# Kernel optimization log

Measured on AMD Instinct MI355X. Metric: run time of the kernel, lower is better.

The kernel has to match this reference:

```python
import jax, jax.numpy as jnp
import numpy as np

BINS = 1024
HEADS = 8
HEAD_DIM = BINS // HEADS          # 128
ROT_DIM = HEAD_DIM // 2           # 64 (rotary applied to first half of head dim)


def depthwise_conv_w(y, kernel):
    # y: (b, c, w, bins); depthwise length-3 conv along frame axis w, pad 1
    b, c, w, g = y.shape
    y2 = y.reshape(b * c, w, g)
    out = jax.lax.conv_general_dilated(
        y2, kernel, window_strides=(1,), padding=((1, 1),),
        dimension_numbers=('NWC', 'WIO', 'NWC'), feature_group_count=g)
    return out.reshape(b, c, w, g)


def rotate_half(x):
    # interleaved pair rotation: (x0,x1) -> (-x1,x0)
    x1 = x[..., ::2]
    x2 = x[..., 1::2]
    return jnp.stack([-x2, x1], axis=-1).reshape(x.shape)


def apply_rotary(t, inv_freq):
    # t: (b, c, H, w, d); rotate first ROT_DIM features along seq axis w
    w = t.shape[-2]
    pos = jnp.arange(w, dtype=t.dtype)
    freqs = pos[:, None] * inv_freq[None, :]        # (w, ROT_DIM//2)
    freqs = jnp.repeat(freqs, 2, axis=-1)           # (w, ROT_DIM)
    cos, sin = jnp.cos(freqs), jnp.sin(freqs)
    t_rot, t_pass = t[..., :ROT_DIM], t[..., ROT_DIM:]
    t_rot = t_rot * cos + rotate_half(t_rot) * sin
    return jnp.concatenate([t_rot, t_pass], axis=-1)


def _qkv(x, W, conv_k):
    # linear over last (bins) dim then depthwise conv over frames, split heads
    y = jnp.einsum('bcwh,gh->bcwg', x, W)
    y = depthwise_conv_w(y, conv_k)
    b, c, w, _ = y.shape
    return y.reshape(b, c, w, HEADS, HEAD_DIM).transpose(0, 1, 3, 2, 4)  # (b,c,H,w,d)


def setup_inputs() -> dict:
    key = jax.random.key(0)
    ks = jax.random.split(key, 8)
    s = 0.02
    inv_freq = (1.0 / (10000.0 ** (np.arange(0, ROT_DIM, 2, dtype=np.float32) / ROT_DIM)))
    return {
        'x': jax.random.normal(ks[0], (2, 2, 1024, BINS), dtype=jnp.float32),
        'q_w': jax.random.normal(ks[1], (BINS, BINS), dtype=jnp.float32) * s,
        'q_conv': jax.random.normal(ks[2], (3, 1, BINS), dtype=jnp.float32) * 0.3,
        'k_w': jax.random.normal(ks[3], (BINS, BINS), dtype=jnp.float32) * s,
        'k_conv': jax.random.normal(ks[4], (3, 1, BINS), dtype=jnp.float32) * 0.3,
        'v_w': jax.random.normal(ks[5], (BINS, BINS), dtype=jnp.float32) * s,
        'v_conv': jax.random.normal(ks[6], (3, 1, BINS), dtype=jnp.float32) * 0.3,
        'out_w': jax.random.normal(ks[7], (BINS, BINS), dtype=jnp.float32) * s,
        'inv_freq': jnp.asarray(inv_freq),
    }


def reference(x, q_w, q_conv, k_w, k_conv, v_w, v_conv, out_w, inv_freq):
    b, c, w, h = x.shape  # h == BINS
    q = apply_rotary(_qkv(x, q_w, q_conv), inv_freq)
    k = apply_rotary(_qkv(x, k_w, k_conv), inv_freq)
    v = _qkv(x, v_w, v_conv)
    scale = 1.0 / jnp.sqrt(jnp.asarray(h, x.dtype))   # NOTE: scale by sqrt(bins), per source
    scores = jnp.einsum('bchqd,bchkd->bchqk', q, k) * scale
    a = jax.nn.softmax(scores, axis=-1)
    o = jnp.einsum('bchqk,bchkd->bchqd', a, v)
    o = o.transpose(0, 1, 3, 2, 4).reshape(b, c, w, h)
    return jnp.einsum('bcwh,gh->bcwg', o, out_w)
```

## Files before the change

### kernel.cpp

```cpp
#include <hip/hip_runtime.h>
#include <stdint.h>

typedef float fv4 __attribute__((ext_vector_type(4)));
typedef float fv2 __attribute__((ext_vector_type(2)));
typedef int   iv4 __attribute__((ext_vector_type(4)));
typedef short sv4 __attribute__((ext_vector_type(4)));
typedef short sv8 __attribute__((ext_vector_type(8)));

__device__ __forceinline__ short f2bf(float f) {
  uint32_t u = __builtin_bit_cast(uint32_t, f);
  u += 0x7FFFu + ((u >> 16) & 1u);
  return (short)(u >> 16);
}
__device__ __forceinline__ float bf2f(short s) {
  uint32_t u = ((uint32_t)(uint16_t)s) << 16;
  return __builtin_bit_cast(float, u);
}
__device__ __forceinline__ float redmax16(float v) {
#pragma unroll
  for (int m = 1; m < 16; m <<= 1) v = fmaxf(v, __shfl_xor(v, m));
  return v;
}
__device__ __forceinline__ float redsum16(float v) {
#pragma unroll
  for (int m = 1; m < 16; m <<= 1) v += __shfl_xor(v, m);
  return v;
}
__device__ __forceinline__ void gload_lds16(const void* g, void* l) {
  __builtin_amdgcn_global_load_lds((const __attribute__((address_space(1))) void*)g,
                                   (__attribute__((address_space(3))) void*)l, 16, 0, 0);
}

__global__ __launch_bounds__(256) void f2bf_k(const float* __restrict__ src,
                                              short* __restrict__ dst) {
  int i = (blockIdx.x * 256 + threadIdx.x) * 4;
  fv4 v = *(const fv4*)(src + i);
  sv4 o;
  o[0] = f2bf(v[0]); o[1] = f2bf(v[1]); o[2] = f2bf(v[2]); o[3] = f2bf(v[3]);
  *(sv4*)(dst + i) = o;
}

__global__ __launch_bounds__(256) void w4_k(const float* __restrict__ s0,
                                            const float* __restrict__ s1,
                                            const float* __restrict__ s2,
                                            const float* __restrict__ s3,
                                            short* __restrict__ dst) {
  int p = blockIdx.x >> 10;
  const float* s = p == 0 ? s0 : (p == 1 ? s1 : (p == 2 ? s2 : s3));
  int i = ((blockIdx.x & 1023) * 256 + threadIdx.x) * 4;
  fv4 v = *(const fv4*)(s + i);
  sv4 o;
  o[0] = f2bf(v[0]); o[1] = f2bf(v[1]); o[2] = f2bf(v[2]); o[3] = f2bf(v[3]);
  *(sv4*)(dst + (size_t)p * 1048576 + i) = o;
}

__global__ __launch_bounds__(256) void ropetab_k(const float* __restrict__ invf,
                                                 fv2* __restrict__ tab) {
  int id = blockIdx.x * 256 + threadIdx.x;
  int w = id >> 5, fi = id & 31;
  float th = (float)w * invf[fi];
  fv2 cs; cs[0] = cosf(th); cs[1] = sinf(th);
  tab[id] = cs;
}

template <typename CT>
__global__ __launch_bounds__(256, 3) void gemm_bt(const short* __restrict__ A,
                                                  const short* __restrict__ B,
                                                  CT* __restrict__ C) {
  __shared__ short As[128 * 64];
  __shared__ short Bs[128 * 64];
  const int tid = threadIdx.x, lane = tid & 63, wid = tid >> 6;
  const int l16 = lane & 15, grp = lane >> 4;
  const int proj = blockIdx.x >> 3;
  const int bn = (blockIdx.x & 7) * 128;
  const int bm = blockIdx.y * 128;
  const short* Bp = B + (size_t)proj * 1048576;
  CT* Cp = C + (size_t)proj * 4194304;
  const int wr = (wid >> 1) * 64, wc = (wid & 1) * 64;
  fv4 acc[4][4] = {};
  const int srow = lane >> 3, scol = (lane & 7) * 8;
  for (int ks = 0; ks < 1024; ks += 64) {
    __syncthreads();
#pragma unroll
    for (int c = 0; c < 4; ++c) {
      int chunk = c * 4 + wid;
      gload_lds16(A + (size_t)(bm + chunk * 8 + srow) * 1024 + ks + scol, As + chunk * 512);
      gload_lds16(Bp + (size_t)(bn + chunk * 8 + srow) * 1024 + ks + scol, Bs + chunk * 512);
    }
    asm volatile("s_waitcnt vmcnt(0)" ::: "memory");
    __syncthreads();
#pragma unroll
    for (int kk = 0; kk < 2; ++kk) {
      sv8 a[4], b[4];
#pragma unroll
      for (int mi = 0; mi < 4; ++mi)
        a[mi] = *(const sv8*)&As[(wr + mi * 16 + l16) * 64 + kk * 32 + grp * 8];
#pragma unroll
      for (int ni = 0; ni < 4; ++ni)
        b[ni] = *(const sv8*)&Bs[(wc + ni * 16 + l16) * 64 + kk * 32 + grp * 8];
#pragma unroll
      for (int mi = 0; mi < 4; ++mi)
#pragma unroll
        for (int ni = 0; ni < 4; ++ni)
          acc[mi][ni] = __builtin_amdgcn_mfma_f32_16x16x32_bf16(a[mi], b[ni], acc[mi][ni], 0, 0, 0);
    }
  }
#pragma unroll
  for (int mi = 0; mi < 4; ++mi)
#pragma unroll
    for (int ni = 0; ni < 4; ++ni)
#pragma unroll
      for (int r = 0; r < 4; ++r) {
        float v = acc[mi][ni][r];
        CT* p = Cp + (size_t)(bm + wr + mi * 16 + grp * 4 + r) * 1024 + bn + wc + ni * 16 + l16;
        if constexpr (sizeof(CT) == 2) *p = f2bf(v); else *p = v;
      }
}

__global__ __launch_bounds__(256) void conv_rope_k(const short* __restrict__ y3,
                                                   const float* __restrict__ cq,
                                                   const float* __restrict__ ckk,
                                                   const float* __restrict__ cv,
                                                   const fv2* __restrict__ tab,
                                                   short* __restrict__ qh,
                                                   short* __restrict__ kh,
                                                   short* __restrict__ vh) {
  const int proj = blockIdx.y;
  const short* y = y3 + (size_t)proj * 4194304;
  const float* ck = proj == 0 ? cq : (proj == 1 ? ckk : cv);
  short* out = proj == 0 ? qh : (proj == 1 ? kh : vh);
  int id = blockIdx.x * 256 + threadIdx.x;
  int g8 = id & 127, w = (id >> 7) & 1023, bc = id >> 17;
  int g0 = g8 << 3;
  const short* row = y + ((size_t)(bc * 1024 + w)) * 1024 + g0;
  float a[8];
  {
    sv8 v = *(const sv8*)row;
    fv4 c0 = *(const fv4*)(ck + 1024 + g0);
    fv4 c1 = *(const fv4*)(ck + 1024 + g0 + 4);
#pragma unroll
    for (int j = 0; j < 4; ++j) { a[j] = bf2f(v[j]) * c0[j]; a[4 + j] = bf2f(v[4 + j]) * c1[j]; }
  }
  if (w > 0) {
    sv8 v = *(const sv8*)(row - 1024);
    fv4 c0 = *(const fv4*)(ck + g0);
    fv4 c1 = *(const fv4*)(ck + g0 + 4);
#pragma unroll
    for (int j = 0; j < 4; ++j) { a[j] += bf2f(v[j]) * c0[j]; a[4 + j] += bf2f(v[4 + j]) * c1[j]; }
  }
  if (w < 1023) {
    sv8 v = *(const sv8*)(row + 1024);
    fv4 c0 = *(const fv4*)(ck + 2048 + g0);
    fv4 c1 = *(const fv4*)(ck + 2048 + g0 + 4);
#pragma unroll
    for (int j = 0; j < 4; ++j) { a[j] += bf2f(v[j]) * c0[j]; a[4 + j] += bf2f(v[4 + j]) * c1[j]; }
  }
  int d0 = g0 & 127;
  if (proj < 2 && d0 < 64) {
#pragma unroll
    for (int jj = 0; jj < 4; ++jj) {
      fv2 cs = tab[(w << 5) + (d0 >> 1) + jj];
      float e0 = a[2 * jj], e1 = a[2 * jj + 1];
      a[2 * jj] = e0 * cs[0] - e1 * cs[1];
      a[2 * jj + 1] = e1 * cs[0] + e0 * cs[1];
    }
  }
  int h = g0 >> 7;
  sv8 o;
#pragma unroll
  for (int j = 0; j < 8; ++j) o[j] = f2bf(a[j]);
  *(sv8*)(out + ((size_t)((bc * 8 + h) * 1024 + w)) * 128 + d0) = o;
}

__global__ __launch_bounds__(256) void vtrans_k(const short* __restrict__ vh,
                                                short* __restrict__ vt) {
  __shared__ short T[64][136];
  const int bch = blockIdx.x, kt = blockIdx.y;
  const short* src = vh + ((size_t)bch * 1024 + kt * 64) * 128;
#pragma unroll
  for (int c = 0; c < 4; ++c) {
    int idx = c * 2048 + threadIdx.x * 8;
    int r = idx >> 7, col = idx & 127;
    *(sv8*)&T[r][col] = *(const sv8*)(src + (size_t)r * 128 + col);
  }
  __syncthreads();
  const int d = threadIdx.x >> 1, half = threadIdx.x & 1;
  short* dst = vt + (size_t)bch * 131072 + (size_t)d * 1024 + kt * 64 + half * 32;
#pragma unroll
  for (int v = 0; v < 4; ++v) {
    sv8 o;
#pragma unroll
    for (int j = 0; j < 8; ++j) o[j] = T[half * 32 + v * 8 + j][d];
    *(sv8*)(dst + v * 8) = o;
  }
}

__global__ __launch_bounds__(256, 1) void attn_k(const short* __restrict__ Q,
                                                 const short* __restrict__ K,
                                                 const short* __restrict__ Vt,
                                                 short* __restrict__ O) {
  __shared__ short Ps[4][32][72];
  const int tid = threadIdx.x, lane = tid & 63, wid = tid >> 6;
  const int l16 = lane & 15, grp = lane >> 4;
  const int bch = blockIdx.x, qb = blockIdx.y;
  const short* Qb = Q + (size_t)bch * 131072;
  const short* Kb = K + (size_t)bch * 131072;
  const short* Vb = Vt + (size_t)bch * 131072;
  const int q0 = qb * 128 + wid * 32;
  sv8 qf[2][4];
#pragma unroll
  for (int mi = 0; mi < 2; ++mi)
#pragma unroll
    for (int kk = 0; kk < 4; ++kk)
      qf[mi][kk] = *(const sv8*)(Qb + (size_t)(q0 + mi * 16 + l16) * 128 + kk * 32 + grp * 8);
  fv4 o[2][8] = {};
  float m[2][4], l[2][4];
#pragma unroll
  for (int mi = 0; mi < 2; ++mi)
#pragma unroll
    for (int r = 0; r < 4; ++r) { m[mi][r] = -1e30f; l[mi][r] = 0.f; }

  for (int kb = 0; kb < 1024; kb += 64) {
    fv4 s[2][4] = {};
    sv8 kf[4][4];
#pragma unroll
    for (int kg = 0; kg < 4; ++kg)
#pragma unroll
      for (int kk = 0; kk < 4; ++kk)
        kf[kg][kk] = *(const sv8*)(Kb + (size_t)(kb + kg * 16 + l16) * 128 + kk * 32 + grp * 8);
#pragma unroll
    for (int kg = 0; kg < 4; ++kg)
#pragma unroll
      for (int kk = 0; kk < 4; ++kk) {
        s[0][kg] = __builtin_amdgcn_mfma_f32_16x16x32_bf16(qf[0][kk], kf[kg][kk], s[0][kg], 0, 0, 0);
        s[1][kg] = __builtin_amdgcn_mfma_f32_16x16x32_bf16(qf[1][kk], kf[kg][kk], s[1][kg], 0, 0, 0);
      }
    sv8 vf[8][2];
#pragma unroll
    for (int db = 0; db < 8; ++db)
#pragma unroll
      for (int ks2 = 0; ks2 < 2; ++ks2)
        vf[db][ks2] = *(const sv8*)(Vb + (size_t)(db * 16 + l16) * 1024 + kb + ks2 * 32 + grp * 8);
    const float sc = 0.03125f;
#pragma unroll
    for (int mi = 0; mi < 2; ++mi) {
      float cor[4];
#pragma unroll
      for (int r = 0; r < 4; ++r) {
#pragma unroll
        for (int kg = 0; kg < 4; ++kg) s[mi][kg][r] *= sc;
        float v0 = fmaxf(fmaxf(s[mi][0][r], s[mi][1][r]), fmaxf(s[mi][2][r], s[mi][3][r]));
        v0 = redmax16(v0);
        float mn = fmaxf(m[mi][r], v0);
        cor[r] = __expf(m[mi][r] - mn);
        m[mi][r] = mn;
        float rs = 0.f;
#pragma unroll
        for (int kg = 0; kg < 4; ++kg) {
          float e = __expf(s[mi][kg][r] - mn);
          s[mi][kg][r] = e;
          rs += e;
        }
        rs = redsum16(rs);
        l[mi][r] = l[mi][r] * cor[r] + rs;
#pragma unroll
        for (int kg = 0; kg < 4; ++kg)
          Ps[wid][mi * 16 + grp * 4 + r][kg * 16 + l16] = f2bf(s[mi][kg][r]);
      }
#pragma unroll
      for (int db = 0; db < 8; ++db)
#pragma unroll
        for (int r = 0; r < 4; ++r) o[mi][db][r] *= cor[r];
    }
    asm volatile("s_waitcnt lgkmcnt(0)" ::: "memory");
    __builtin_amdgcn_sched_barrier(0);
#pragma unroll
    for (int mi = 0; mi < 2; ++mi) {
      sv8 pa0 = *(const sv8*)&Ps[wid][mi * 16 + l16][grp * 8];
      sv8 pa1 = *(const sv8*)&Ps[wid][mi * 16 + l16][32 + grp * 8];
#pragma unroll
      for (int db = 0; db < 8; ++db) {
        o[mi][db] = __builtin_amdgcn_mfma_f32_16x16x32_bf16(pa0, vf[db][0], o[mi][db], 0, 0, 0);
        o[mi][db] = __builtin_amdgcn_mfma_f32_16x16x32_bf16(pa1, vf[db][1], o[mi][db], 0, 0, 0);
      }
    }
  }
  const int bc = bch >> 3, h = bch & 7;
#pragma unroll
  for (int mi = 0; mi < 2; ++mi) {
    float inv[4];
#pragma unroll
    for (int r = 0; r < 4; ++r) inv[r] = 1.0f / l[mi][r];
#pragma unroll
    for (int db = 0; db < 8; ++db)
#pragma unroll
      for (int r = 0; r < 4; ++r) {
        int q = q0 + mi * 16 + grp * 4 + r;
        O[((size_t)(bc * 1024 + q)) * 1024 + h * 128 + db * 16 + l16] =
            f2bf(o[mi][db][r] * inv[r]);
      }
  }
}

extern "C" void kernel_launch(void* const* d_in, const int* in_sizes, int n_in,
                              void* d_out, int out_size, void* d_ws, size_t ws_size,
                              hipStream_t stream) {
  const float* x = (const float*)d_in[0];
  const float* q_w = (const float*)d_in[1];
  const float* q_conv = (const float*)d_in[2];
  const float* k_w = (const float*)d_in[3];
  const float* k_conv = (const float*)d_in[4];
  const float* v_w = (const float*)d_in[5];
  const float* v_conv = (const float*)d_in[6];
  const float* out_w = (const float*)d_in[7];
  const float* inv_freq = (const float*)d_in[8];

  char* ws = (char*)d_ws;
  short* x_bf = (short*)(ws);
  short* w4   = (short*)(ws + 8388608);
  fv2*   tab  = (fv2*)(ws + 16777216);
  short* y3   = (short*)(ws + 17301504);
  short* q_h  = (short*)(ws);
  short* k_h  = (short*)(ws + 42467328);
  short* v_h  = (short*)(ws + 50855936);
  short* v_t  = (short*)(ws + 17301504);
  short* o_fl = (short*)(ws + 25690112);

  f2bf_k<<<4096, 256, 0, stream>>>(x, x_bf);
  w4_k<<<4096, 256, 0, stream>>>(q_w, k_w, v_w, out_w, w4);
  ropetab_k<<<128, 256, 0, stream>>>(inv_freq, tab);

  gemm_bt<short><<<dim3(24, 32), 256, 0, stream>>>(x_bf, w4, y3);
  conv_rope_k<<<dim3(2048, 3), 256, 0, stream>>>(y3, q_conv, k_conv, v_conv, tab, q_h, k_h, v_h);
  vtrans_k<<<dim3(32, 16), 256, 0, stream>>>(v_h, v_t);
  attn_k<<<dim3(32, 8), 256, 0, stream>>>(q_h, k_h, v_t, o_fl);
  gemm_bt<float><<<dim3(8, 32), 256, 0, stream>>>(o_fl, w4 + 3145728, (float*)d_out);
}
```

Measured before the change: 233.4 us.

## Split attention KV range across waves and merge partial softmax in LDS

Each block now handles 32 queries with its four waves splitting the 1024 keys into four 256-key chunks, instead of each wave owning 32 queries over all keys. Partial max and sum statistics plus the output accumulators are combined through shared memory with a tree reduction, and the grid grows from 256 to 1024 blocks with launch bounds raised to 3. The aim is better CU occupancy and latency hiding on a GPU with many CUs. In exchange it adds LDS traffic, extra barriers and a reduction epilogue, and each K/V tile is now loaded by four times as many blocks.

```diff
diff --git a/kernel.cpp b/kernel.cpp
--- a/kernel.cpp
+++ b/kernel.cpp
@@ -195,18 +195,21 @@
   }
 }
 
-__global__ __launch_bounds__(256, 1) void attn_k(const short* __restrict__ Q,
+__global__ __launch_bounds__(256, 3) void attn_k(const short* __restrict__ Q,
                                                  const short* __restrict__ K,
                                                  const short* __restrict__ Vt,
                                                  short* __restrict__ O) {
   __shared__ short Ps[4][32][72];
+  __shared__ float Lml[4][2][32];
+  __shared__ float Ob[2][32][132];
   const int tid = threadIdx.x, lane = tid & 63, wid = tid >> 6;
   const int l16 = lane & 15, grp = lane >> 4;
   const int bch = blockIdx.x, qb = blockIdx.y;
   const short* Qb = Q + (size_t)bch * 131072;
   const short* Kb = K + (size_t)bch * 131072;
   const short* Vb = Vt + (size_t)bch * 131072;
-  const int q0 = qb * 128 + wid * 32;
+  const int q0 = qb * 32;
+  const int kv0 = wid * 256;
   sv8 qf[2][4];
 #pragma unroll
   for (int mi = 0; mi < 2; ++mi)
@@ -220,7 +223,8 @@
 #pragma unroll
     for (int r = 0; r < 4; ++r) { m[mi][r] = -1e30f; l[mi][r] = 0.f; }
 
-  for (int kb = 0; kb < 1024; kb += 64) {
+  for (int ki = 0; ki < 4; ++ki) {
+    const int kb = kv0 + ki * 64;
     fv4 s[2][4] = {};
     sv8 kf[4][4];
 #pragma unroll
@@ -285,20 +289,84 @@
       }
     }
   }
-  const int bc = bch >> 3, h = bch & 7;
-#pragma unroll
-  for (int mi = 0; mi < 2; ++mi) {
-    float inv[4];
-#pragma unroll
-    for (int r = 0; r < 4; ++r) inv[r] = 1.0f / l[mi][r];
-#pragma unroll
-    for (int db = 0; db < 8; ++db)
+
+  const int rowb = grp * 4;
+  if (l16 == 0) {
+#pragma unroll
+    for (int mi = 0; mi < 2; ++mi)
 #pragma unroll
       for (int r = 0; r < 4; ++r) {
-        int q = q0 + mi * 16 + grp * 4 + r;
-        O[((size_t)(bc * 1024 + q)) * 1024 + h * 128 + db * 16 + l16] =
-            f2bf(o[mi][db][r] * inv[r]);
+        Lml[wid][0][mi * 16 + rowb + r] = m[mi][r];
+        Lml[wid][1][mi * 16 + rowb + r] = l[mi][r];
       }
+  }
+  __syncthreads();
+  float Lfin[2][4];
+#pragma unroll
+  for (int mi = 0; mi < 2; ++mi)
+#pragma unroll
+    for (int r = 0; r < 4; ++r) {
+      int row = mi * 16 + rowb + r;
+      float m0 = Lml[0][0][row], m1 = Lml[1][0][row];
+      float m2 = Lml[2][0][row], m3 = Lml[3][0][row];
+      float M = fmaxf(fmaxf(m0, m1), fmaxf(m2, m3));
+      float a0 = __expf(m0 - M), a1 = __expf(m1 - M);
+      float a2 = __expf(m2 - M), a3 = __expf(m3 - M);
+      Lfin[mi][r] = a0 * Lml[0][1][row] + a1 * Lml[1][1][row] +
+                    a2 * Lml[2][1][row] + a3 * Lml[3][1][row];
+      float aw = (wid == 0) ? a0 : ((wid == 1) ? a1 : ((wid == 2) ? a2 : a3));
+#pragma unroll
+      for (int db = 0; db < 8; ++db) o[mi][db][r] *= aw;
+    }
+  if (wid == 1 || wid == 3) {
+    const int b = wid >> 1;
+#pragma unroll
+    for (int mi = 0; mi < 2; ++mi)
+#pragma unroll
+      for (int db = 0; db < 8; ++db)
+#pragma unroll
+        for (int r = 0; r < 4; ++r)
+          Ob[b][mi * 16 + rowb + r][db * 16 + l16] = o[mi][db][r];
+  }
+  __syncthreads();
+  if (wid == 0 || wid == 2) {
+    const int b = wid >> 1;
+#pragma unroll
+    for (int mi = 0; mi < 2; ++mi)
+#pragma unroll
+      for (int db = 0; db < 8; ++db)
+#pragma unroll
+        for (int r = 0; r < 4; ++r)
+          o[mi][db][r] += Ob[b][mi * 16 + rowb + r][db * 16 + l16];
+  }
+  __syncthreads();
+  if (wid == 2) {
+#pragma unroll
+    for (int mi = 0; mi < 2; ++mi)
+#pragma unroll
+      for (int db = 0; db < 8; ++db)
+#pragma unroll
+        for (int r = 0; r < 4; ++r)
+          Ob[0][mi * 16 + rowb + r][db * 16 + l16] = o[mi][db][r];
+  }
+  __syncthreads();
+  if (wid == 0) {
+    const int bc = bch >> 3, h = bch & 7;
+#pragma unroll
+    for (int mi = 0; mi < 2; ++mi) {
+      float inv[4];
+#pragma unroll
+      for (int r = 0; r < 4; ++r) inv[r] = 1.0f / Lfin[mi][r];
+#pragma unroll
+      for (int db = 0; db < 8; ++db)
+#pragma unroll
+        for (int r = 0; r < 4; ++r) {
+          float v = o[mi][db][r] + Ob[0][mi * 16 + rowb + r][db * 16 + l16];
+          int q = q0 + mi * 16 + rowb + r;
+          O[((size_t)(bc * 1024 + q)) * 1024 + h * 128 + db * 16 + l16] =
+              f2bf(v * inv[r]);
+        }
+    }
   }
 }
 
@@ -333,6 +401,6 @@
   gemm_bt<short><<<dim3(24, 32), 256, 0, stream>>>(x_bf, w4, y3);
   conv_rope_k<<<dim3(2048, 3), 256, 0, stream>>>(y3, q_conv, k_conv, v_conv, tab, q_h, k_h, v_h);
   vtrans_k<<<dim3(32, 16), 256, 0, stream>>>(v_h, v_t);
-  attn_k<<<dim3(32, 8), 256, 0, stream>>>(q_h, k_h, v_t, o_fl);
+  attn_k<<<dim3(32, 32), 256, 0, stream>>>(q_h, k_h, v_t, o_fl);
   gemm_bt<float><<<dim3(8, 32), 256, 0, stream>>>(o_fl, w4 + 3145728, (float*)d_out);
 }
```

Measured after the change: 281.3 us. +20.5%, slower.
